# Performance work log

Hardware: AMD Instinct MI355X
Metric: run time of the kernel (lower is better)

The kernel has to match this reference:

```python
import jax, jax.numpy as jnp
import numpy as np

EPS_BN = 1e-5


def _batchnorm(h, g, b):
    # training-mode BatchNorm1d over the flattened (B*N*k) axis
    mu = jnp.mean(h, axis=0)
    var = jnp.var(h, axis=0)
    return g * (h - mu) * jax.lax.rsqrt(var + EPS_BN) + b


def setup_inputs() -> dict:
    key = jax.random.key(0)
    ks = jax.random.split(key, 5)
    B, N = 4, 8192
    x = jax.random.normal(ks[0], (B, N, 3), dtype=jnp.float32)
    W1 = jax.random.normal(ks[1], (7, 10), dtype=jnp.float32) * (1.0 / np.sqrt(7.0))
    b1 = jax.random.normal(ks[2], (10,), dtype=jnp.float32) * 0.01
    W2 = jax.random.normal(ks[3], (10, 10), dtype=jnp.float32) * (1.0 / np.sqrt(10.0))
    b2 = jax.random.normal(ks[4], (10,), dtype=jnp.float32) * 0.01
    g1 = jnp.ones((10,), jnp.float32); be1 = jnp.zeros((10,), jnp.float32)
    g2 = jnp.ones((10,), jnp.float32); be2 = jnp.zeros((10,), jnp.float32)
    return {"x": x, "W1": W1, "b1": b1, "g1": g1, "be1": be1,
            "W2": W2, "b2": b2, "g2": g2, "be2": be2, "k": 9}


def reference(x, W1, b1, g1, be1, W2, b2, g2, be2, k):
    B, N, C = x.shape
    # --- kNN graph (brute force, self included as nearest) ---
    sq = jnp.sum(x * x, axis=-1)                                    # (B,N)
    d2 = sq[:, :, None] + sq[:, None, :] - 2.0 * jnp.einsum('bnc,bmc->bnm', x, x)
    _, idx = jax.lax.top_k(-d2, k + 1)                              # (B,N,k+1)
    nbrs = x[jnp.arange(B)[:, None, None], idx]                     # (B,N,k+1,3)
    rel = (nbrs - x[:, :, None, :])[:, :, 1:, :]                    # drop self -> (B,N,k,3)
    # --- sort neighbors by azimuth phi = atan2(y, x) ---
    phi = jnp.arctan2(rel[..., 1], rel[..., 0])                     # (B,N,k)
    order = jnp.argsort(phi, axis=-1)
    v1 = jnp.take_along_axis(rel, order[..., None], axis=2)         # (B,N,k,3)
    v2 = jnp.roll(v1, -1, axis=2)                                   # next neighbor (cyclic)
    # --- umbrella-style surface features ---
    centroids = 0.5 * (v1 + v2)
    normals = jnp.cross(v1, v2)
    normals = normals / (jnp.linalg.norm(normals, axis=-1, keepdims=True) + 1e-6)
    sign = jnp.where(normals[..., 0:1, 0] > 0, 1.0, -1.0)[..., None]  # (B,N,1,1)
    normals = normals * sign
    position = jnp.sum(normals * centroids, axis=-1, keepdims=True) / jnp.sqrt(jnp.asarray(3.0, x.dtype))
    feat = jnp.concatenate([centroids, normals, position], axis=-1)   # (B,N,k,7)
    feat = feat.reshape(B * N * k, 7)
    # --- tiny MLP + max-pool over k ---
    h = jax.nn.relu(_batchnorm(feat @ W1 + b1, g1, be1))
    h = jax.nn.relu(_batchnorm(h @ W2 + b2, g2, be2))
    return jnp.max(h.reshape(B, N, k, 10), axis=2)                  # (B,N,10)
```

## Files before the change

kernel.cpp:

```cpp
#include <hip/hip_runtime.h>
#include <math.h>
#include <float.h>
#include <stdint.h>

#define B_ 4
#define N_ 8192
#define K_ 9
#define NPTS (B_ * N_)
#define NROWS (NPTS * K_)
#define SPLIT 8
#define CHUNK (N_ / SPLIT)
#define NGROUP 32
#define GSIZE (CHUNK / NGROUP)
#define GSTRIDE 33
#define NCOPY 16

typedef float f4 __attribute__((ext_vector_type(4)));
typedef float f32x2 __attribute__((ext_vector_type(2)));

__device__ __forceinline__ f32x2 dist2_pk(f32x2 xx, f32x2 yy, f32x2 zz, f32x2 ww,
                                          f32x2 qx, f32x2 qy, f32x2 qz, f32x2 qw) {
  f32x2 t0 = qx * xx;
  f32x2 t1 = __builtin_elementwise_fma(qy, yy, t0);
  f32x2 t2 = __builtin_elementwise_fma(qz, zz, t1);
  f32x2 s  = qw + ww;
  f32x2 m2 = {-2.0f, -2.0f};
  return __builtin_elementwise_fma(t2, m2, s);
}

#define GDECL(G) float gd##G; int gi##G;
#define TOURN8()                                                           \
  float e01d, e23d, e45d, e67d, f03d, f47d, md;                            \
  int   e01i, e23i, e45i, e67i, f03i, f47i, mi;                            \
  { bool t;                                                                \
    t = d1 < d0; e01d = t ? d1 : d0; e01i = t ? (j + 1) : (j + 0);         \
    t = d3 < d2; e23d = t ? d3 : d2; e23i = t ? (j + 3) : (j + 2);         \
    t = d5 < d4; e45d = t ? d5 : d4; e45i = t ? (j + 5) : (j + 4);         \
    t = d7 < d6; e67d = t ? d7 : d6; e67i = t ? (j + 7) : (j + 6);         \
    t = e23d < e01d; f03d = t ? e23d : e01d; f03i = t ? e23i : e01i;       \
    t = e67d < e45d; f47d = t ? e67d : e45d; f47i = t ? e67i : e45i;       \
    t = f47d < f03d; md = t ? f47d : f03d; mi = t ? f47i : f03i; }
#define SCANG(G)                                                           \
  { float bgd = FLT_MAX; int bgi = 0;                                      \
    _Pragma("clang loop unroll(disable)")                                  \
    for (int pr = 0; pr < 16; pr += 4) {                                   \
      const f4* cp = CH + (G * GSTRIDE + 2 * pr);                          \
      f4 A0 = cp[0], B0 = cp[1], A1 = cp[2], B1 = cp[3];                   \
      f4 A2 = cp[4], B2 = cp[5], A3 = cp[6], B3 = cp[7];                   \
      int j = G * GSIZE + 2 * pr;                                          \
      f32x2 dA = dist2_pk(__builtin_shufflevector(A0, A0, 0, 1),           \
                          __builtin_shufflevector(A0, A0, 2, 3),           \
                          __builtin_shufflevector(B0, B0, 0, 1),           \
                          __builtin_shufflevector(B0, B0, 2, 3),           \
                          qx2, qy2, qz2, qw2);                             \
      f32x2 dB = dist2_pk(__builtin_shufflevector(A1, A1, 0, 1),           \
                          __builtin_shufflevector(A1, A1, 2, 3),           \
                          __builtin_shufflevector(B1, B1, 0, 1),           \
                          __builtin_shufflevector(B1, B1, 2, 3),           \
                          qx2, qy2, qz2, qw2);                             \
      f32x2 dC = dist2_pk(__builtin_shufflevector(A2, A2, 0, 1),           \
                          __builtin_shufflevector(A2, A2, 2, 3),           \
                          __builtin_shufflevector(B2, B2, 0, 1),           \
                          __builtin_shufflevector(B2, B2, 2, 3),           \
                          qx2, qy2, qz2, qw2);                             \
      f32x2 dD = dist2_pk(__builtin_shufflevector(A3, A3, 0, 1),           \
                          __builtin_shufflevector(A3, A3, 2, 3),           \
                          __builtin_shufflevector(B3, B3, 0, 1),           \
                          __builtin_shufflevector(B3, B3, 2, 3),           \
                          qx2, qy2, qz2, qw2);                             \
      float d0 = dA.x, d1 = dA.y, d2 = dB.x, d3 = dB.y;                    \
      float d4 = dC.x, d5 = dC.y, d6 = dD.x, d7 = dD.y;                    \
      if (HS) {                                                            \
        d0 = (j + 0 == nl) ? FLT_MAX : d0;                                 \
        d1 = (j + 1 == nl) ? FLT_MAX : d1;                                 \
        d2 = (j + 2 == nl) ? FLT_MAX : d2;                                 \
        d3 = (j + 3 == nl) ? FLT_MAX : d3;                                 \
        d4 = (j + 4 == nl) ? FLT_MAX : d4;                                 \
        d5 = (j + 5 == nl) ? FLT_MAX : d5;                                 \
        d6 = (j + 6 == nl) ? FLT_MAX : d6;                                 \
        d7 = (j + 7 == nl) ? FLT_MAX : d7;                                 \
      }                                                                    \
      TOURN8();                                                            \
      bool lt = md < bgd; bgd = lt ? md : bgd; bgi = lt ? mi : bgi;        \
    }                                                                      \
    gd##G = bgd; gi##G = bgi; }
#define LMC(G, S)                                                          \
  { bool lt = gd##G < wd##S;                                               \
    wd##S = lt ? gd##G : wd##S; wi##S = lt ? gi##G : wi##S;                \
    wg##S = lt ? G : wg##S; }
#define CMB(S)                                                             \
  { bool lt = wd##S < wda;                                                 \
    wda = lt ? wd##S : wda; wia = lt ? wi##S : wia; wga = lt ? wg##S : wga; }
#define WBK(G)                                                             \
  { bool m = (wg == G); gd##G = m ? nd : gd##G; gi##G = m ? ni : gi##G; }

template <bool HS>
__device__ __forceinline__ void knn_chunk(const f4* CH, f32x2 qx2, f32x2 qy2,
                                          f32x2 qz2, f32x2 qw2,
                                          int nl, int j0, int s, int p,
                                          uint2* __restrict__ PBDI) {
  GDECL(0) GDECL(1) GDECL(2) GDECL(3) GDECL(4) GDECL(5) GDECL(6) GDECL(7)
  GDECL(8) GDECL(9) GDECL(10) GDECL(11) GDECL(12) GDECL(13) GDECL(14) GDECL(15)
  GDECL(16) GDECL(17) GDECL(18) GDECL(19) GDECL(20) GDECL(21) GDECL(22) GDECL(23)
  GDECL(24) GDECL(25) GDECL(26) GDECL(27) GDECL(28) GDECL(29) GDECL(30) GDECL(31)

  SCANG(0) SCANG(1) SCANG(2) SCANG(3) SCANG(4) SCANG(5) SCANG(6) SCANG(7)
  SCANG(8) SCANG(9) SCANG(10) SCANG(11) SCANG(12) SCANG(13) SCANG(14) SCANG(15)
  SCANG(16) SCANG(17) SCANG(18) SCANG(19) SCANG(20) SCANG(21) SCANG(22) SCANG(23)
  SCANG(24) SCANG(25) SCANG(26) SCANG(27) SCANG(28) SCANG(29) SCANG(30) SCANG(31)

#pragma clang loop unroll(disable)
  for (int r = 0; r < K_; ++r) {
    float wda = gd0; int wia = gi0; int wga = 0;
    LMC(1,a) LMC(2,a) LMC(3,a) LMC(4,a) LMC(5,a) LMC(6,a) LMC(7,a)
    float wdb = gd8; int wib = gi8; int wgb = 8;
    LMC(9,b) LMC(10,b) LMC(11,b) LMC(12,b) LMC(13,b) LMC(14,b) LMC(15,b)
    float wdc = gd16; int wic = gi16; int wgc = 16;
    LMC(17,c) LMC(18,c) LMC(19,c) LMC(20,c) LMC(21,c) LMC(22,c) LMC(23,c)
    float wdd = gd24; int wid = gi24; int wgd = 24;
    LMC(25,d) LMC(26,d) LMC(27,d) LMC(28,d) LMC(29,d) LMC(30,d) LMC(31,d)
    CMB(b) CMB(c) CMB(d)
    float wd = wda; int wi = wia; int wg = wga;

    uint2 o; o.x = __float_as_uint(wd); o.y = (unsigned)(j0 + wi);
    PBDI[(size_t)(s * K_ + r) * NPTS + p] = o;

    int ab = wg * GSTRIDE;
    int jb = wg * GSIZE;
    float nd = FLT_MAX; int ni = 0;
#pragma clang loop unroll(disable)
    for (int pr = 0; pr < 16; pr += 4) {
      const f4* cp = CH + (ab + 2 * pr);
      f4 A0 = cp[0], B0 = cp[1], A1 = cp[2], B1 = cp[3];
      f4 A2 = cp[4], B2 = cp[5], A3 = cp[6], B3 = cp[7];
      int j = jb + 2 * pr;
      f32x2 dA = dist2_pk(__builtin_shufflevector(A0, A0, 0, 1),
                          __builtin_shufflevector(A0, A0, 2, 3),
                          __builtin_shufflevector(B0, B0, 0, 1),
                          __builtin_shufflevector(B0, B0, 2, 3),
                          qx2, qy2, qz2, qw2);
      f32x2 dB = dist2_pk(__builtin_shufflevector(A1, A1, 0, 1),
                          __builtin_shufflevector(A1, A1, 2, 3),
                          __builtin_shufflevector(B1, B1, 0, 1),
                          __builtin_shufflevector(B1, B1, 2, 3),
                          qx2, qy2, qz2, qw2);
      f32x2 dC = dist2_pk(__builtin_shufflevector(A2, A2, 0, 1),
                          __builtin_shufflevector(A2, A2, 2, 3),
                          __builtin_shufflevector(B2, B2, 0, 1),
                          __builtin_shufflevector(B2, B2, 2, 3),
                          qx2, qy2, qz2, qw2);
      f32x2 dD = dist2_pk(__builtin_shufflevector(A3, A3, 0, 1),
                          __builtin_shufflevector(A3, A3, 2, 3),
                          __builtin_shufflevector(B3, B3, 0, 1),
                          __builtin_shufflevector(B3, B3, 2, 3),
                          qx2, qy2, qz2, qw2);
      float d0 = dA.x, d1 = dA.y, d2 = dB.x, d3 = dB.y;
      float d4 = dC.x, d5 = dC.y, d6 = dD.x, d7 = dD.y;
      if (HS) {
        d0 = (j + 0 == nl) ? FLT_MAX : d0;
        d1 = (j + 1 == nl) ? FLT_MAX : d1;
        d2 = (j + 2 == nl) ? FLT_MAX : d2;
        d3 = (j + 3 == nl) ? FLT_MAX : d3;
        d4 = (j + 4 == nl) ? FLT_MAX : d4;
        d5 = (j + 5 == nl) ? FLT_MAX : d5;
        d6 = (j + 6 == nl) ? FLT_MAX : d6;
        d7 = (j + 7 == nl) ? FLT_MAX : d7;
      }
      bool k0 = (d0 > wd) | ((d0 == wd) & ((j + 0) > wi));
      bool k1 = (d1 > wd) | ((d1 == wd) & ((j + 1) > wi));
      bool k2 = (d2 > wd) | ((d2 == wd) & ((j + 2) > wi));
      bool k3 = (d3 > wd) | ((d3 == wd) & ((j + 3) > wi));
      bool k4 = (d4 > wd) | ((d4 == wd) & ((j + 4) > wi));
      bool k5 = (d5 > wd) | ((d5 == wd) & ((j + 5) > wi));
      bool k6 = (d6 > wd) | ((d6 == wd) & ((j + 6) > wi));
      bool k7 = (d7 > wd) | ((d7 == wd) & ((j + 7) > wi));
      d0 = k0 ? d0 : FLT_MAX;
      d1 = k1 ? d1 : FLT_MAX;
      d2 = k2 ? d2 : FLT_MAX;
      d3 = k3 ? d3 : FLT_MAX;
      d4 = k4 ? d4 : FLT_MAX;
      d5 = k5 ? d5 : FLT_MAX;
      d6 = k6 ? d6 : FLT_MAX;
      d7 = k7 ? d7 : FLT_MAX;
      TOURN8();
      bool lt = md < nd; nd = lt ? md : nd; ni = lt ? mi : ni;
    }
    WBK(0) WBK(1) WBK(2) WBK(3) WBK(4) WBK(5) WBK(6) WBK(7)
    WBK(8) WBK(9) WBK(10) WBK(11) WBK(12) WBK(13) WBK(14) WBK(15)
    WBK(16) WBK(17) WBK(18) WBK(19) WBK(20) WBK(21) WBK(22) WBK(23)
    WBK(24) WBK(25) WBK(26) WBK(27) WBK(28) WBK(29) WBK(30) WBK(31)
  }
}

__launch_bounds__(128, 4)
__global__ void k_knn(const float* __restrict__ x, uint2* __restrict__ PBDI) {
  __shared__ f4 CH[NGROUP * GSTRIDE];
  int bid = blockIdx.x;
  int pg = bid >> 3;
  int s = bid & (SPLIT - 1);
  int p = pg * 128 + threadIdx.x;
  int b = p >> 13;
  int n = p & (N_ - 1);
  int bO = b * N_;
  int j0 = s * CHUNK;

  const float* xq = x + 3 * (size_t)p;
  float qa = xq[0], qb = xq[1], qc = xq[2];
  float qw = qa * qa + qb * qb + qc * qc;
  f32x2 qx2 = {qa, qa}, qy2 = {qb, qb}, qz2 = {qc, qc}, qw2 = {qw, qw};

  for (int u = threadIdx.x; u < CHUNK / 2; u += 128) {
    const float* xp = x + 3 * (size_t)(bO + j0 + 2 * u);
    float a0 = xp[0], b0 = xp[1], c0 = xp[2];
    float a1 = xp[3], b1 = xp[4], c1 = xp[5];
    int G = u >> 4, rr = u & 15;
    f4 lo = {a0, a1, b0, b1};
    f4 hi = {c0, c1, a0 * a0 + b0 * b0 + c0 * c0, a1 * a1 + b1 * b1 + c1 * c1};
    CH[G * GSTRIDE + 2 * rr] = lo;
    CH[G * GSTRIDE + 2 * rr + 1] = hi;
  }
  __syncthreads();

  int n0 = (pg * 128) & (N_ - 1);
  int nl = n - j0;
  if (s == (n0 >> 10)) knn_chunk<true >(CH, qx2, qy2, qz2, qw2, nl, j0, s, p, PBDI);
  else                 knn_chunk<false>(CH, qx2, qy2, qz2, qw2, nl, j0, s, p, PBDI);
}

#define LVL(bdv, biv)                                                     \
  { bool lt = cd < (bdv); float td = (bdv); int ti = (biv);               \
    (bdv) = lt ? cd : (bdv); (biv) = lt ? ci : (biv);                     \
    cd = lt ? td : cd; ci = lt ? ti : ci; }
#define INS9ALL()                                                         \
  LVL(b0d, b0i) LVL(b1d, b1i) LVL(b2d, b2i) LVL(b3d, b3i) LVL(b4d, b4i)  \
  LVL(b5d, b5i) LVL(b6d, b6i) LVL(b7d, b7i) LVL(b8d, b8i)
#define TOP9_DECL()                                                       \
  float b0d = FLT_MAX, b1d = FLT_MAX, b2d = FLT_MAX, b3d = FLT_MAX,       \
        b4d = FLT_MAX, b5d = FLT_MAX, b6d = FLT_MAX, b7d = FLT_MAX,       \
        b8d = FLT_MAX;                                                    \
  int b0i = 0, b1i = 0, b2i = 0, b3i = 0, b4i = 0, b5i = 0, b6i = 0,      \
      b7i = 0, b8i = 0;

#define MKREL(T)                                                          \
  float rx##T, ry##T, rz##T, ph##T;                                       \
  { const float* mp = x + 3 * (size_t)(bO + b##T##i);                     \
    rx##T = mp[0] - qa; ry##T = mp[1] - qb; rz##T = mp[2] - qc;           \
    ph##T = atan2f(ry##T, rx##T); }

#define CE(A, Bv)                                                         \
  { bool lt = ph##Bv < ph##A; float t0;                                   \
    t0 = ph##A; ph##A = lt ? ph##Bv : t0; ph##Bv = lt ? t0 : ph##Bv;      \
    t0 = rx##A; rx##A = lt ? rx##Bv : t0; rx##Bv = lt ? t0 : rx##Bv;      \
    t0 = ry##A; ry##A = lt ? ry##Bv : t0; ry##Bv = lt ? t0 : ry##Bv;      \
    t0 = rz##A; rz##A = lt ? rz##Bv : t0; rz##Bv = lt ? t0 : rz##Bv; }

#define ST9(arr, v0, v1, v2, v3, v4, v5, v6, v7, v8)                      \
  arr[0 * 64 + pl] = v0; arr[1 * 64 + pl] = v1; arr[2 * 64 + pl] = v2;    \
  arr[3 * 64 + pl] = v3; arr[4 * 64 + pl] = v4; arr[5 * 64 + pl] = v5;    \
  arr[6 * 64 + pl] = v6; arr[7 * 64 + pl] = v7; arr[8 * 64 + pl] = v8;

__launch_bounds__(256, 4)
__global__ void k_tail1(const float* __restrict__ x, const uint2* __restrict__ PBDI,
                        const float* __restrict__ W1, const float* __restrict__ b1,
                        float* __restrict__ H1, double* __restrict__ ACC) {
  __shared__ float  LMD[64 * 37];
  __shared__ int    LMI[64 * 37];
  __shared__ float  LREL[3][9 * 64];
  __shared__ float  LSGN[64];
  __shared__ double sred[4][20];

  int q = threadIdx.x >> 6;
  int pl = threadIdx.x & 63;
  int pbase = blockIdx.x * 64;
  int p = pbase + pl;

  {
    TOP9_DECL();
#pragma clang loop unroll_count(2)
    for (int e = 0; e < 2 * K_; ++e) {
      uint2 v = PBDI[(size_t)(q * 2 * K_ + e) * NPTS + p];
      float cd = __uint_as_float(v.x);
      int ci = (int)v.y;
      INS9ALL();
    }
    int base = pl * 37 + q * 9;
    LMD[base + 0] = b0d; LMD[base + 1] = b1d; LMD[base + 2] = b2d;
    LMD[base + 3] = b3d; LMD[base + 4] = b4d; LMD[base + 5] = b5d;
    LMD[base + 6] = b6d; LMD[base + 7] = b7d; LMD[base + 8] = b8d;
    LMI[base + 0] = b0i; LMI[base + 1] = b1i; LMI[base + 2] = b2i;
    LMI[base + 3] = b3i; LMI[base + 4] = b4i; LMI[base + 5] = b5i;
    LMI[base + 6] = b6i; LMI[base + 7] = b7i; LMI[base + 8] = b8i;
  }
  __syncthreads();

  if (q == 0) {
    int b = p >> 13;
    int bO = b * N_;
    const float* xq = x + 3 * (size_t)p;
    float qa = xq[0], qb = xq[1], qc = xq[2];

    TOP9_DECL();
#pragma clang loop unroll_count(3)
    for (int e = 0; e < 4 * K_; ++e) {
      float cd = LMD[pl * 37 + e];
      int ci = LMI[pl * 37 + e];
      INS9ALL();
    }

    MKREL(0) MKREL(1) MKREL(2) MKREL(3) MKREL(4)
    MKREL(5) MKREL(6) MKREL(7) MKREL(8)

    CE(0,1)
    CE(1,2) CE(0,1)
    CE(2,3) CE(1,2) CE(0,1)
    CE(3,4) CE(2,3) CE(1,2) CE(0,1)
    CE(4,5) CE(3,4) CE(2,3) CE(1,2) CE(0,1)
    CE(5,6) CE(4,5) CE(3,4) CE(2,3) CE(1,2) CE(0,1)
    CE(6,7) CE(5,6) CE(4,5) CE(3,4) CE(2,3) CE(1,2) CE(0,1)
    CE(7,8) CE(6,7) CE(5,6) CE(4,5) CE(3,4) CE(2,3) CE(1,2) CE(0,1)

    float nx0 = ry0 * rz1 - rz0 * ry1;
    float ny0 = rz0 * rx1 - rx0 * rz1;
    float nz0 = rx0 * ry1 - ry0 * rx1;
    float nrm0 = sqrtf(nx0 * nx0 + ny0 * ny0 + nz0 * nz0) + 1e-6f;
    LSGN[pl] = ((nx0 / nrm0) > 0.0f) ? 1.0f : -1.0f;

    ST9(LREL[0], rx0, rx1, rx2, rx3, rx4, rx5, rx6, rx7, rx8)
    ST9(LREL[1], ry0, ry1, ry2, ry3, ry4, ry5, ry6, ry7, ry8)
    ST9(LREL[2], rz0, rz1, rz2, rz3, rz4, rz5, rz6, rz7, rz8)
  }
  __syncthreads();

  double sum[10], ss[10];
#pragma unroll
  for (int c = 0; c < 10; ++c) { sum[c] = 0.0; ss[c] = 0.0; }

#pragma clang loop unroll(disable)
  for (int rl = threadIdx.x; rl < 9 * 64; rl += 256) {
    int t = rl >> 6;
    int pp = rl & 63;
    int t2 = (t + 1 == K_) ? 0 : t + 1;
    float v1x = LREL[0][t * 64 + pp];
    float v1y = LREL[1][t * 64 + pp];
    float v1z = LREL[2][t * 64 + pp];
    float v2x = LREL[0][t2 * 64 + pp];
    float v2y = LREL[1][t2 * 64 + pp];
    float v2z = LREL[2][t2 * 64 + pp];
    float sgn = LSGN[pp];

    float cx = 0.5f * (v1x + v2x);
    float cy = 0.5f * (v1y + v2y);
    float cz = 0.5f * (v1z + v2z);
    float nx = v1y * v2z - v1z * v2y;
    float ny = v1z * v2x - v1x * v2z;
    float nz = v1x * v2y - v1y * v2x;
    float nrm = sqrtf(nx * nx + ny * ny + nz * nz) + 1e-6f;
    nx /= nrm; ny /= nrm; nz /= nrm;
    nx *= sgn; ny *= sgn; nz *= sgn;
    float pos = (nx * cx + ny * cy + nz * cz) / 1.7320508075688772f;

    float fv[7] = {cx, cy, cz, nx, ny, nz, pos};
#pragma unroll
    for (int c = 0; c < 10; ++c) {
      float h = b1[c];
#pragma unroll
      for (int rr = 0; rr < 7; ++rr) h = fmaf(fv[rr], W1[rr * 10 + c], h);
      H1[(size_t)c * NROWS + (size_t)t * NPTS + pbase + pp] = h;
      double hd = (double)h;
      sum[c] += hd; ss[c] += hd * hd;
    }
  }

  int lane = threadIdx.x & 63, wv = threadIdx.x >> 6;
#pragma unroll
  for (int c = 0; c < 10; ++c) {
    double a = sum[c];
#pragma unroll
    for (int off = 32; off > 0; off >>= 1) a += __shfl_down(a, off);
    if (lane == 0) sred[wv][c] = a;
    double qq = ss[c];
#pragma unroll
    for (int off = 32; off > 0; off >>= 1) qq += __shfl_down(qq, off);
    if (lane == 0) sred[wv][10 + c] = qq;
  }
  __syncthreads();
  if (threadIdx.x < 20) {
    atomicAdd(&ACC[(blockIdx.x & (NCOPY - 1)) * 40 + threadIdx.x],
              sred[0][threadIdx.x] + sred[1][threadIdx.x] +
              sred[2][threadIdx.x] + sred[3][threadIdx.x]);
  }
}

__launch_bounds__(256)
__global__ void k_mlp2(const float* __restrict__ H1, double* __restrict__ ACC,
                       const float* __restrict__ g1, const float* __restrict__ be1,
                       const float* __restrict__ W2, const float* __restrict__ b2,
                       float* __restrict__ H2) {
  __shared__ float MR[20];
  if (threadIdx.x < 10) {
    double s0 = 0.0, s1 = 0.0;
#pragma unroll
    for (int cc = 0; cc < NCOPY; ++cc) {
      s0 += ACC[cc * 40 + threadIdx.x];
      s1 += ACC[cc * 40 + 10 + threadIdx.x];
    }
    double mu = s0 / (double)NROWS;
    double var = s1 / (double)NROWS - mu * mu;
    MR[threadIdx.x] = (float)mu;
    MR[10 + threadIdx.x] = (float)(1.0 / sqrt(var + 1e-5));
  }
  __syncthreads();

  int r = blockIdx.x * 256 + threadIdx.x;
  float v[10];
#pragma unroll
  for (int c = 0; c < 10; ++c) {
    float h = H1[(size_t)c * NROWS + r];
    float z = g1[c] * (h - MR[c]) * MR[10 + c] + be1[c];
    v[c] = z > 0.0f ? z : 0.0f;
  }
  float o[10];
#pragma unroll
  for (int c = 0; c < 10; ++c) {
    float h = b2[c];
#pragma unroll
    for (int t = 0; t < 10; ++t) h = fmaf(v[t], W2[t * 10 + c], h);
    o[c] = h;
    H2[(size_t)c * NROWS + r] = h;
  }

  __shared__ double sred[4][20];
  int lane = threadIdx.x & 63, wv = threadIdx.x >> 6;
#pragma unroll
  for (int c = 0; c < 10; ++c) {
    double a = (double)o[c];
#pragma unroll
    for (int off = 32; off > 0; off >>= 1) a += __shfl_down(a, off);
    if (lane == 0) sred[wv][c] = a;
    double qq = (double)o[c] * (double)o[c];
#pragma unroll
    for (int off = 32; off > 0; off >>= 1) qq += __shfl_down(qq, off);
    if (lane == 0) sred[wv][10 + c] = qq;
  }
  __syncthreads();
  if (threadIdx.x < 20) {
    atomicAdd(&ACC[(blockIdx.x & (NCOPY - 1)) * 40 + 20 + threadIdx.x],
              sred[0][threadIdx.x] + sred[1][threadIdx.x] +
              sred[2][threadIdx.x] + sred[3][threadIdx.x]);
  }
}

__launch_bounds__(256)
__global__ void k_out(const float* __restrict__ H2, const double* __restrict__ ACC,
                      const float* __restrict__ g2, const float* __restrict__ be2,
                      float* __restrict__ out) {
  __shared__ float MR[20];
  if (threadIdx.x < 10) {
    double s0 = 0.0, s1 = 0.0;
#pragma unroll
    for (int cc = 0; cc < NCOPY; ++cc) {
      s0 += ACC[cc * 40 + 20 + threadIdx.x];
      s1 += ACC[cc * 40 + 30 + threadIdx.x];
    }
    double mu = s0 / (double)NROWS;
    double var = s1 / (double)NROWS - mu * mu;
    MR[threadIdx.x] = (float)mu;
    MR[10 + threadIdx.x] = (float)(1.0 / sqrt(var + 1e-5));
  }
  __syncthreads();

  int p = blockIdx.x * 256 + threadIdx.x;
#pragma unroll
  for (int c = 0; c < 10; ++c) {
    float m = -FLT_MAX;
#pragma unroll
    for (int j = 0; j < K_; ++j) {
      float h = H2[(size_t)c * NROWS + j * NPTS + p];
      float z = g2[c] * (h - MR[c]) * MR[10 + c] + be2[c];
      z = z > 0.0f ? z : 0.0f;
      m = fmaxf(m, z);
    }
    out[(size_t)p * 10 + c] = m;
  }
}

extern "C" void kernel_launch(void* const* d_in, const int* in_sizes, int n_in,
                              void* d_out, int out_size, void* d_ws, size_t ws_size,
                              hipStream_t stream) {
  (void)in_sizes; (void)n_in; (void)out_size; (void)ws_size;
  const float* x  = (const float*)d_in[0];
  const float* W1 = (const float*)d_in[1];
  const float* b1 = (const float*)d_in[2];
  const float* g1 = (const float*)d_in[3];
  const float* be1= (const float*)d_in[4];
  const float* W2 = (const float*)d_in[5];
  const float* b2 = (const float*)d_in[6];
  const float* g2 = (const float*)d_in[7];
  const float* be2= (const float*)d_in[8];
  float* out = (float*)d_out;

  char* base = (char*)d_ws;
  uint2*  PBDI = (uint2*)base;
  float*  H1 = (float*)(base + (size_t)SPLIT * K_ * NPTS * 8);
  double* ACC = (double*)(H1 + (size_t)10 * NROWS);
  float*  H2 = (float*)PBDI;

  hipMemsetAsync(ACC, 0, NCOPY * 40 * sizeof(double), stream);
  k_knn<<<(NPTS / 128) * SPLIT, 128, 0, stream>>>(x, PBDI);
  k_tail1<<<NPTS / 64, 256, 0, stream>>>(x, PBDI, W1, b1, H1, ACC);
  k_mlp2<<<NROWS / 256, 256, 0, stream>>>(H1, ACC, g1, be1, W2, b2, H2);
  k_out<<<NPTS / 256, 256, 0, stream>>>(H2, ACC, g2, be2, out);
}
```

Baseline: 236.5 us.

## Drop index tracking from kNN group scan and cache winner-group distances in registers

The first-pass group scan now keeps only the minimum distance per group, using fminf with no index tournament. In each extraction round the winning group's distances are recomputed once into 32 registers. The index is recovered as the lowest index matching the minimum, and the refill tournament reuses those cached values instead of a second LDS pass. The output kernel is also relaunched with 64-thread blocks, and the BN-statistics setup is split across 20 threads. This cuts ALU work in the dominant scan, at the cost of register pressure and extra compare work in each round.

```diff
diff --git a/kernel.cpp b/kernel.cpp
--- a/kernel.cpp
+++ b/kernel.cpp
@@ -18,6 +18,9 @@
 typedef float f4 __attribute__((ext_vector_type(4)));
 typedef float f32x2 __attribute__((ext_vector_type(2)));
 
+#define SH(V, a, b) __builtin_shufflevector(V, V, a, b)
+#define IMIN(a, b) (((a) < (b)) ? (a) : (b))
+
 __device__ __forceinline__ f32x2 dist2_pk(f32x2 xx, f32x2 yy, f32x2 zz, f32x2 ww,
                                           f32x2 qx, f32x2 qy, f32x2 qz, f32x2 qw) {
   f32x2 t0 = qx * xx;
@@ -29,6 +32,91 @@
 }
 
 #define GDECL(G) float gd##G; int gi##G;
+
+#define SCANG(G)                                                           \
+  { float bgd = FLT_MAX;                                                   \
+    _Pragma("clang loop unroll(disable)")                                  \
+    for (int pr = 0; pr < 16; pr += 4) {                                   \
+      const f4* cp = CH + (G * GSTRIDE + 2 * pr);                          \
+      f4 A0 = cp[0], B0 = cp[1], A1 = cp[2], B1 = cp[3];                   \
+      f4 A2 = cp[4], B2 = cp[5], A3 = cp[6], B3 = cp[7];                   \
+      f32x2 dA = dist2_pk(SH(A0,0,1), SH(A0,2,3), SH(B0,0,1), SH(B0,2,3),  \
+                          qx2, qy2, qz2, qw2);                             \
+      f32x2 dB = dist2_pk(SH(A1,0,1), SH(A1,2,3), SH(B1,0,1), SH(B1,2,3),  \
+                          qx2, qy2, qz2, qw2);                             \
+      f32x2 dC = dist2_pk(SH(A2,0,1), SH(A2,2,3), SH(B2,0,1), SH(B2,2,3),  \
+                          qx2, qy2, qz2, qw2);                             \
+      f32x2 dD = dist2_pk(SH(A3,0,1), SH(A3,2,3), SH(B3,0,1), SH(B3,2,3),  \
+                          qx2, qy2, qz2, qw2);                             \
+      float d0 = dA.x, d1 = dA.y, d2 = dB.x, d3 = dB.y;                    \
+      float d4 = dC.x, d5 = dC.y, d6 = dD.x, d7 = dD.y;                    \
+      if (HS) {                                                            \
+        int j = G * GSIZE + 2 * pr;                                        \
+        d0 = (j + 0 == nl) ? FLT_MAX : d0;                                 \
+        d1 = (j + 1 == nl) ? FLT_MAX : d1;                                 \
+        d2 = (j + 2 == nl) ? FLT_MAX : d2;                                 \
+        d3 = (j + 3 == nl) ? FLT_MAX : d3;                                 \
+        d4 = (j + 4 == nl) ? FLT_MAX : d4;                                 \
+        d5 = (j + 5 == nl) ? FLT_MAX : d5;                                 \
+        d6 = (j + 6 == nl) ? FLT_MAX : d6;                                 \
+        d7 = (j + 7 == nl) ? FLT_MAX : d7;                                 \
+      }                                                                    \
+      float m = fminf(fminf(fminf(d0, d1), fminf(d2, d3)),                 \
+                      fminf(fminf(d4, d5), fminf(d6, d7)));                \
+      bgd = fminf(bgd, m);                                                 \
+    }                                                                      \
+    gd##G = bgd; gi##G = -1; }
+
+#define LMC(G, S)                                                          \
+  { bool lt = gd##G < wd##S;                                               \
+    wd##S = lt ? gd##G : wd##S; wi##S = lt ? gi##G : wi##S;                \
+    wg##S = lt ? G : wg##S; }
+#define CMB(S)                                                             \
+  { bool lt = wd##S < wda;                                                 \
+    wda = lt ? wd##S : wda; wia = lt ? wi##S : wia; wga = lt ? wg##S : wga; }
+#define WBK(G)                                                             \
+  { bool m = (wg == G); gd##G = m ? nd : gd##G; gi##G = m ? ni : gi##G; }
+
+#define RESC(T, OFS)                                                       \
+  { const f4* cp = CH + (ab + OFS);                                        \
+    f4 A0 = cp[0], B0 = cp[1], A1 = cp[2], B1 = cp[3];                     \
+    f4 A2 = cp[4], B2 = cp[5], A3 = cp[6], B3 = cp[7];                     \
+    f32x2 dA = dist2_pk(SH(A0,0,1), SH(A0,2,3), SH(B0,0,1), SH(B0,2,3),    \
+                        qx2, qy2, qz2, qw2);                               \
+    f32x2 dB = dist2_pk(SH(A1,0,1), SH(A1,2,3), SH(B1,0,1), SH(B1,2,3),    \
+                        qx2, qy2, qz2, qw2);                               \
+    f32x2 dC = dist2_pk(SH(A2,0,1), SH(A2,2,3), SH(B2,0,1), SH(B2,2,3),    \
+                        qx2, qy2, qz2, qw2);                               \
+    f32x2 dD = dist2_pk(SH(A3,0,1), SH(A3,2,3), SH(B3,0,1), SH(B3,2,3),    \
+                        qx2, qy2, qz2, qw2);                               \
+    rc##T##0 = dA.x; rc##T##1 = dA.y; rc##T##2 = dB.x; rc##T##3 = dB.y;    \
+    rc##T##4 = dC.x; rc##T##5 = dC.y; rc##T##6 = dD.x; rc##T##7 = dD.y;    \
+    if (HS) {                                                              \
+      int j = jb + OFS;                                                    \
+      rc##T##0 = (j + 0 == nl) ? FLT_MAX : rc##T##0;                       \
+      rc##T##1 = (j + 1 == nl) ? FLT_MAX : rc##T##1;                       \
+      rc##T##2 = (j + 2 == nl) ? FLT_MAX : rc##T##2;                       \
+      rc##T##3 = (j + 3 == nl) ? FLT_MAX : rc##T##3;                       \
+      rc##T##4 = (j + 4 == nl) ? FLT_MAX : rc##T##4;                       \
+      rc##T##5 = (j + 5 == nl) ? FLT_MAX : rc##T##5;                       \
+      rc##T##6 = (j + 6 == nl) ? FLT_MAX : rc##T##6;                       \
+      rc##T##7 = (j + 7 == nl) ? FLT_MAX : rc##T##7;                       \
+    } }
+
+#define MT8(T, OFS)                                                        \
+  { int j = jb + OFS;                                                      \
+    int a0 = (rc##T##0 == wd) ? (j + 0) : 0x7fffffff;                      \
+    int a1 = (rc##T##1 == wd) ? (j + 1) : 0x7fffffff;                      \
+    int a2 = (rc##T##2 == wd) ? (j + 2) : 0x7fffffff;                      \
+    int a3 = (rc##T##3 == wd) ? (j + 3) : 0x7fffffff;                      \
+    int a4 = (rc##T##4 == wd) ? (j + 4) : 0x7fffffff;                      \
+    int a5 = (rc##T##5 == wd) ? (j + 5) : 0x7fffffff;                      \
+    int a6 = (rc##T##6 == wd) ? (j + 6) : 0x7fffffff;                      \
+    int a7 = (rc##T##7 == wd) ? (j + 7) : 0x7fffffff;                      \
+    int mA = IMIN(IMIN(a0, a1), IMIN(a2, a3));                             \
+    int mB = IMIN(IMIN(a4, a5), IMIN(a6, a7));                             \
+    jm = IMIN(jm, IMIN(mA, mB)); }
+
 #define TOURN8()                                                           \
   float e01d, e23d, e45d, e67d, f03d, f47d, md;                            \
   int   e01i, e23i, e45i, e67i, f03i, f47i, mi;                            \
@@ -40,59 +128,29 @@
     t = e23d < e01d; f03d = t ? e23d : e01d; f03i = t ? e23i : e01i;       \
     t = e67d < e45d; f47d = t ? e67d : e45d; f47i = t ? e67i : e45i;       \
     t = f47d < f03d; md = t ? f47d : f03d; mi = t ? f47i : f03i; }
-#define SCANG(G)                                                           \
-  { float bgd = FLT_MAX; int bgi = 0;                                      \
-    _Pragma("clang loop unroll(disable)")                                  \
-    for (int pr = 0; pr < 16; pr += 4) {                                   \
-      const f4* cp = CH + (G * GSTRIDE + 2 * pr);                          \
-      f4 A0 = cp[0], B0 = cp[1], A1 = cp[2], B1 = cp[3];                   \
-      f4 A2 = cp[4], B2 = cp[5], A3 = cp[6], B3 = cp[7];                   \
-      int j = G * GSIZE + 2 * pr;                                          \
-      f32x2 dA = dist2_pk(__builtin_shufflevector(A0, A0, 0, 1),           \
-                          __builtin_shufflevector(A0, A0, 2, 3),           \
-                          __builtin_shufflevector(B0, B0, 0, 1),           \
-                          __builtin_shufflevector(B0, B0, 2, 3),           \
-                          qx2, qy2, qz2, qw2);                             \
-      f32x2 dB = dist2_pk(__builtin_shufflevector(A1, A1, 0, 1),           \
-                          __builtin_shufflevector(A1, A1, 2, 3),           \
-                          __builtin_shufflevector(B1, B1, 0, 1),           \
-                          __builtin_shufflevector(B1, B1, 2, 3),           \
-                          qx2, qy2, qz2, qw2);                             \
-      f32x2 dC = dist2_pk(__builtin_shufflevector(A2, A2, 0, 1),           \
-                          __builtin_shufflevector(A2, A2, 2, 3),           \
-                          __builtin_shufflevector(B2, B2, 0, 1),           \
-                          __builtin_shufflevector(B2, B2, 2, 3),           \
-                          qx2, qy2, qz2, qw2);                             \
-      f32x2 dD = dist2_pk(__builtin_shufflevector(A3, A3, 0, 1),           \
-                          __builtin_shufflevector(A3, A3, 2, 3),           \
-                          __builtin_shufflevector(B3, B3, 0, 1),           \
-                          __builtin_shufflevector(B3, B3, 2, 3),           \
-                          qx2, qy2, qz2, qw2);                             \
-      float d0 = dA.x, d1 = dA.y, d2 = dB.x, d3 = dB.y;                    \
-      float d4 = dC.x, d5 = dC.y, d6 = dD.x, d7 = dD.y;                    \
-      if (HS) {                                                            \
-        d0 = (j + 0 == nl) ? FLT_MAX : d0;                                 \
-        d1 = (j + 1 == nl) ? FLT_MAX : d1;                                 \
-        d2 = (j + 2 == nl) ? FLT_MAX : d2;                                 \
-        d3 = (j + 3 == nl) ? FLT_MAX : d3;                                 \
-        d4 = (j + 4 == nl) ? FLT_MAX : d4;                                 \
-        d5 = (j + 5 == nl) ? FLT_MAX : d5;                                 \
-        d6 = (j + 6 == nl) ? FLT_MAX : d6;                                 \
-        d7 = (j + 7 == nl) ? FLT_MAX : d7;                                 \
-      }                                                                    \
-      TOURN8();                                                            \
-      bool lt = md < bgd; bgd = lt ? md : bgd; bgi = lt ? mi : bgi;        \
-    }                                                                      \
-    gd##G = bgd; gi##G = bgi; }
-#define LMC(G, S)                                                          \
-  { bool lt = gd##G < wd##S;                                               \
-    wd##S = lt ? gd##G : wd##S; wi##S = lt ? gi##G : wi##S;                \
-    wg##S = lt ? G : wg##S; }
-#define CMB(S)                                                             \
-  { bool lt = wd##S < wda;                                                 \
-    wda = lt ? wd##S : wda; wia = lt ? wi##S : wia; wga = lt ? wg##S : wga; }
-#define WBK(G)                                                             \
-  { bool m = (wg == G); gd##G = m ? nd : gd##G; gi##G = m ? ni : gi##G; }
+
+#define RF(T, OFS)                                                         \
+  { float d0 = rc##T##0, d1 = rc##T##1, d2 = rc##T##2, d3 = rc##T##3;      \
+    float d4 = rc##T##4, d5 = rc##T##5, d6 = rc##T##6, d7 = rc##T##7;      \
+    int j = jb + OFS;                                                      \
+    bool k0 = (d0 > wd) | ((d0 == wd) & ((j + 0) > wi));                   \
+    bool k1 = (d1 > wd) | ((d1 == wd) & ((j + 1) > wi));                   \
+    bool k2 = (d2 > wd) | ((d2 == wd) & ((j + 2) > wi));                   \
+    bool k3 = (d3 > wd) | ((d3 == wd) & ((j + 3) > wi));                   \
+    bool k4 = (d4 > wd) | ((d4 == wd) & ((j + 4) > wi));                   \
+    bool k5 = (d5 > wd) | ((d5 == wd) & ((j + 5) > wi));                   \
+    bool k6 = (d6 > wd) | ((d6 == wd) & ((j + 6) > wi));                   \
+    bool k7 = (d7 > wd) | ((d7 == wd) & ((j + 7) > wi));                   \
+    d0 = k0 ? d0 : FLT_MAX;                                                \
+    d1 = k1 ? d1 : FLT_MAX;                                                \
+    d2 = k2 ? d2 : FLT_MAX;                                                \
+    d3 = k3 ? d3 : FLT_MAX;                                                \
+    d4 = k4 ? d4 : FLT_MAX;                                                \
+    d5 = k5 ? d5 : FLT_MAX;                                                \
+    d6 = k6 ? d6 : FLT_MAX;                                                \
+    d7 = k7 ? d7 : FLT_MAX;                                                \
+    TOURN8();                                                              \
+    bool lt = md < nd; nd = lt ? md : nd; ni = lt ? mi : ni; }
 
 template <bool HS>
 __device__ __forceinline__ void knn_chunk(const f4* CH, f32x2 qx2, f32x2 qy2,
@@ -120,71 +178,27 @@
     float wdd = gd24; int wid = gi24; int wgd = 24;
     LMC(25,d) LMC(26,d) LMC(27,d) LMC(28,d) LMC(29,d) LMC(30,d) LMC(31,d)
     CMB(b) CMB(c) CMB(d)
-    float wd = wda; int wi = wia; int wg = wga;
+    float wd = wda; int wist = wia; int wg = wga;
+
+    int ab = wg * GSTRIDE;
+    int jb = wg * GSIZE;
+
+    float rcA0, rcA1, rcA2, rcA3, rcA4, rcA5, rcA6, rcA7;
+    float rcB0, rcB1, rcB2, rcB3, rcB4, rcB5, rcB6, rcB7;
+    float rcC0, rcC1, rcC2, rcC3, rcC4, rcC5, rcC6, rcC7;
+    float rcD0, rcD1, rcD2, rcD3, rcD4, rcD5, rcD6, rcD7;
+    RESC(A, 0) RESC(B, 8) RESC(C, 16) RESC(D, 24)
+
+    int jm = 0x7fffffff;
+    MT8(A, 0) MT8(B, 8) MT8(C, 16) MT8(D, 24)
+    int wi = (wist >= 0) ? wist : jm;
 
     uint2 o; o.x = __float_as_uint(wd); o.y = (unsigned)(j0 + wi);
     PBDI[(size_t)(s * K_ + r) * NPTS + p] = o;
 
-    int ab = wg * GSTRIDE;
-    int jb = wg * GSIZE;
     float nd = FLT_MAX; int ni = 0;
-#pragma clang loop unroll(disable)
-    for (int pr = 0; pr < 16; pr += 4) {
-      const f4* cp = CH + (ab + 2 * pr);
-      f4 A0 = cp[0], B0 = cp[1], A1 = cp[2], B1 = cp[3];
-      f4 A2 = cp[4], B2 = cp[5], A3 = cp[6], B3 = cp[7];
-      int j = jb + 2 * pr;
-      f32x2 dA = dist2_pk(__builtin_shufflevector(A0, A0, 0, 1),
-                          __builtin_shufflevector(A0, A0, 2, 3),
-                          __builtin_shufflevector(B0, B0, 0, 1),
-                          __builtin_shufflevector(B0, B0, 2, 3),
-                          qx2, qy2, qz2, qw2);
-      f32x2 dB = dist2_pk(__builtin_shufflevector(A1, A1, 0, 1),
-                          __builtin_shufflevector(A1, A1, 2, 3),
-                          __builtin_shufflevector(B1, B1, 0, 1),
-                          __builtin_shufflevector(B1, B1, 2, 3),
-                          qx2, qy2, qz2, qw2);
-      f32x2 dC = dist2_pk(__builtin_shufflevector(A2, A2, 0, 1),
-                          __builtin_shufflevector(A2, A2, 2, 3),
-                          __builtin_shufflevector(B2, B2, 0, 1),
-                          __builtin_shufflevector(B2, B2, 2, 3),
-                          qx2, qy2, qz2, qw2);
-      f32x2 dD = dist2_pk(__builtin_shufflevector(A3, A3, 0, 1),
-                          __builtin_shufflevector(A3, A3, 2, 3),
-                          __builtin_shufflevector(B3, B3, 0, 1),
-                          __builtin_shufflevector(B3, B3, 2, 3),
-                          qx2, qy2, qz2, qw2);
-      float d0 = dA.x, d1 = dA.y, d2 = dB.x, d3 = dB.y;
-      float d4 = dC.x, d5 = dC.y, d6 = dD.x, d7 = dD.y;
-      if (HS) {
-        d0 = (j + 0 == nl) ? FLT_MAX : d0;
-        d1 = (j + 1 == nl) ? FLT_MAX : d1;
-        d2 = (j + 2 == nl) ? FLT_MAX : d2;
-        d3 = (j + 3 == nl) ? FLT_MAX : d3;
-        d4 = (j + 4 == nl) ? FLT_MAX : d4;
-        d5 = (j + 5 == nl) ? FLT_MAX : d5;
-        d6 = (j + 6 == nl) ? FLT_MAX : d6;
-        d7 = (j + 7 == nl) ? FLT_MAX : d7;
-      }
-      bool k0 = (d0 > wd) | ((d0 == wd) & ((j + 0) > wi));
-      bool k1 = (d1 > wd) | ((d1 == wd) & ((j + 1) > wi));
-      bool k2 = (d2 > wd) | ((d2 == wd) & ((j + 2) > wi));
-      bool k3 = (d3 > wd) | ((d3 == wd) & ((j + 3) > wi));
-      bool k4 = (d4 > wd) | ((d4 == wd) & ((j + 4) > wi));
-      bool k5 = (d5 > wd) | ((d5 == wd) & ((j + 5) > wi));
-      bool k6 = (d6 > wd) | ((d6 == wd) & ((j + 6) > wi));
-      bool k7 = (d7 > wd) | ((d7 == wd) & ((j + 7) > wi));
-      d0 = k0 ? d0 : FLT_MAX;
-      d1 = k1 ? d1 : FLT_MAX;
-      d2 = k2 ? d2 : FLT_MAX;
-      d3 = k3 ? d3 : FLT_MAX;
-      d4 = k4 ? d4 : FLT_MAX;
-      d5 = k5 ? d5 : FLT_MAX;
-      d6 = k6 ? d6 : FLT_MAX;
-      d7 = k7 ? d7 : FLT_MAX;
-      TOURN8();
-      bool lt = md < nd; nd = lt ? md : nd; ni = lt ? mi : ni;
-    }
+    RF(A, 0) RF(B, 8) RF(C, 16) RF(D, 24)
+
     WBK(0) WBK(1) WBK(2) WBK(3) WBK(4) WBK(5) WBK(6) WBK(7)
     WBK(8) WBK(9) WBK(10) WBK(11) WBK(12) WBK(13) WBK(14) WBK(15)
     WBK(16) WBK(17) WBK(18) WBK(19) WBK(20) WBK(21) WBK(22) WBK(23)
@@ -450,26 +464,27 @@
   }
 }
 
-__launch_bounds__(256)
+__launch_bounds__(64)
 __global__ void k_out(const float* __restrict__ H2, const double* __restrict__ ACC,
                       const float* __restrict__ g2, const float* __restrict__ be2,
                       float* __restrict__ out) {
   __shared__ float MR[20];
-  if (threadIdx.x < 10) {
+  if (threadIdx.x < 20) {
+    int c = threadIdx.x % 10;
+    int half = threadIdx.x / 10;
     double s0 = 0.0, s1 = 0.0;
 #pragma unroll
     for (int cc = 0; cc < NCOPY; ++cc) {
-      s0 += ACC[cc * 40 + 20 + threadIdx.x];
-      s1 += ACC[cc * 40 + 30 + threadIdx.x];
+      s0 += ACC[cc * 40 + 20 + c];
+      s1 += ACC[cc * 40 + 30 + c];
     }
     double mu = s0 / (double)NROWS;
     double var = s1 / (double)NROWS - mu * mu;
-    MR[threadIdx.x] = (float)mu;
-    MR[10 + threadIdx.x] = (float)(1.0 / sqrt(var + 1e-5));
-  }
-  __syncthreads();
-
-  int p = blockIdx.x * 256 + threadIdx.x;
+    MR[threadIdx.x] = half ? (float)(1.0 / sqrt(var + 1e-5)) : (float)mu;
+  }
+  __syncthreads();
+
+  int p = blockIdx.x * 64 + threadIdx.x;
 #pragma unroll
   for (int c = 0; c < 10; ++c) {
     float m = -FLT_MAX;
@@ -509,5 +524,5 @@
   k_knn<<<(NPTS / 128) * SPLIT, 128, 0, stream>>>(x, PBDI);
   k_tail1<<<NPTS / 64, 256, 0, stream>>>(x, PBDI, W1, b1, H1, ACC);
   k_mlp2<<<NROWS / 256, 256, 0, stream>>>(H1, ACC, g1, be1, W2, b2, H2);
-  k_out<<<NPTS / 256, 256, 0, stream>>>(H2, ACC, g2, be2, out);
-}
+  k_out<<<NPTS / 64, 64, 0, stream>>>(H2, ACC, g2, be2, out);
+}
```

Result: no change. 235.7 us (-0.3%).

## Reduce max over k before second BatchNorm using monotonicity and gamma sign

Applied to the files above, without the earlier changes.

k_mlp2 now processes one point per thread, iterates over its k neighbor rows, and keeps a running max (or min when gamma2 is negative) of the pre-BN layer-2 outputs. Only these per-point extremes are written, instead of the full k-row H2 tensor. k_out then applies BN+ReLU to a single value per channel. This relies on BN+ReLU being monotone in h with direction set by the sign of gamma, and it removes most of the H2 write and reread traffic. The cost is smaller 64-thread blocks and a serial per-thread loop over k.

```diff
diff --git a/kernel.cpp b/kernel.cpp
--- a/kernel.cpp
+++ b/kernel.cpp
@@ -391,96 +391,107 @@
   }
 }
 
-__launch_bounds__(256)
+__launch_bounds__(64)
 __global__ void k_mlp2(const float* __restrict__ H1, double* __restrict__ ACC,
                        const float* __restrict__ g1, const float* __restrict__ be1,
                        const float* __restrict__ W2, const float* __restrict__ b2,
-                       float* __restrict__ H2) {
+                       const float* __restrict__ g2, float* __restrict__ EXT) {
   __shared__ float MR[20];
-  if (threadIdx.x < 10) {
+  __shared__ double sred[20];
+  if (threadIdx.x < 20) {
+    int c = threadIdx.x % 10;
+    int half = threadIdx.x / 10;
     double s0 = 0.0, s1 = 0.0;
 #pragma unroll
     for (int cc = 0; cc < NCOPY; ++cc) {
-      s0 += ACC[cc * 40 + threadIdx.x];
-      s1 += ACC[cc * 40 + 10 + threadIdx.x];
+      s0 += ACC[cc * 40 + c];
+      s1 += ACC[cc * 40 + 10 + c];
     }
     double mu = s0 / (double)NROWS;
     double var = s1 / (double)NROWS - mu * mu;
-    MR[threadIdx.x] = (float)mu;
-    MR[10 + threadIdx.x] = (float)(1.0 / sqrt(var + 1e-5));
-  }
-  __syncthreads();
-
-  int r = blockIdx.x * 256 + threadIdx.x;
-  float v[10];
+    MR[threadIdx.x] = half ? (float)(1.0 / sqrt(var + 1e-5)) : (float)mu;
+  }
+  __syncthreads();
+
+  int p = blockIdx.x * 64 + threadIdx.x;
+  double sum[10], ss[10];
+  float ext[10], sg[10];
 #pragma unroll
   for (int c = 0; c < 10; ++c) {
-    float h = H1[(size_t)c * NROWS + r];
-    float z = g1[c] * (h - MR[c]) * MR[10 + c] + be1[c];
-    v[c] = z > 0.0f ? z : 0.0f;
-  }
-  float o[10];
+    sum[c] = 0.0; ss[c] = 0.0;
+    sg[c] = g2[c];
+    ext[c] = (sg[c] >= 0.0f) ? -FLT_MAX : FLT_MAX;
+  }
+
+#pragma clang loop unroll(disable)
+  for (int t = 0; t < K_; ++t) {
+    float v[10];
+#pragma unroll
+    for (int c = 0; c < 10; ++c) {
+      float h = H1[(size_t)c * NROWS + (size_t)t * NPTS + p];
+      float z = g1[c] * (h - MR[c]) * MR[10 + c] + be1[c];
+      v[c] = z > 0.0f ? z : 0.0f;
+    }
+#pragma unroll
+    for (int c = 0; c < 10; ++c) {
+      float h = b2[c];
+#pragma unroll
+      for (int u = 0; u < 10; ++u) h = fmaf(v[u], W2[u * 10 + c], h);
+      sum[c] += (double)h;
+      ss[c] += (double)h * (double)h;
+      ext[c] = (sg[c] >= 0.0f) ? fmaxf(ext[c], h) : fminf(ext[c], h);
+    }
+  }
+
+#pragma unroll
+  for (int c = 0; c < 10; ++c)
+    EXT[(size_t)c * NPTS + p] = ext[c];
+
 #pragma unroll
   for (int c = 0; c < 10; ++c) {
-    float h = b2[c];
-#pragma unroll
-    for (int t = 0; t < 10; ++t) h = fmaf(v[t], W2[t * 10 + c], h);
-    o[c] = h;
-    H2[(size_t)c * NROWS + r] = h;
-  }
-
-  __shared__ double sred[4][20];
-  int lane = threadIdx.x & 63, wv = threadIdx.x >> 6;
-#pragma unroll
-  for (int c = 0; c < 10; ++c) {
-    double a = (double)o[c];
+    double a = sum[c];
 #pragma unroll
     for (int off = 32; off > 0; off >>= 1) a += __shfl_down(a, off);
-    if (lane == 0) sred[wv][c] = a;
-    double qq = (double)o[c] * (double)o[c];
+    if (threadIdx.x == 0) sred[c] = a;
+    double qq = ss[c];
 #pragma unroll
     for (int off = 32; off > 0; off >>= 1) qq += __shfl_down(qq, off);
-    if (lane == 0) sred[wv][10 + c] = qq;
+    if (threadIdx.x == 0) sred[10 + c] = qq;
   }
   __syncthreads();
   if (threadIdx.x < 20) {
     atomicAdd(&ACC[(blockIdx.x & (NCOPY - 1)) * 40 + 20 + threadIdx.x],
-              sred[0][threadIdx.x] + sred[1][threadIdx.x] +
-              sred[2][threadIdx.x] + sred[3][threadIdx.x]);
-  }
-}
-
-__launch_bounds__(256)
-__global__ void k_out(const float* __restrict__ H2, const double* __restrict__ ACC,
+              sred[threadIdx.x]);
+  }
+}
+
+__launch_bounds__(64)
+__global__ void k_out(const float* __restrict__ EXT, const double* __restrict__ ACC,
                       const float* __restrict__ g2, const float* __restrict__ be2,
                       float* __restrict__ out) {
   __shared__ float MR[20];
-  if (threadIdx.x < 10) {
+  if (threadIdx.x < 20) {
+    int c = threadIdx.x % 10;
+    int half = threadIdx.x / 10;
     double s0 = 0.0, s1 = 0.0;
 #pragma unroll
     for (int cc = 0; cc < NCOPY; ++cc) {
-      s0 += ACC[cc * 40 + 20 + threadIdx.x];
-      s1 += ACC[cc * 40 + 30 + threadIdx.x];
+      s0 += ACC[cc * 40 + 20 + c];
+      s1 += ACC[cc * 40 + 30 + c];
     }
     double mu = s0 / (double)NROWS;
     double var = s1 / (double)NROWS - mu * mu;
-    MR[threadIdx.x] = (float)mu;
-    MR[10 + threadIdx.x] = (float)(1.0 / sqrt(var + 1e-5));
-  }
-  __syncthreads();
-
-  int p = blockIdx.x * 256 + threadIdx.x;
+    MR[threadIdx.x] = half ? (float)(1.0 / sqrt(var + 1e-5)) : (float)mu;
+  }
+  __syncthreads();
+
+  int p = blockIdx.x * 64 + threadIdx.x;
 #pragma unroll
   for (int c = 0; c < 10; ++c) {
-    float m = -FLT_MAX;
-#pragma unroll
-    for (int j = 0; j < K_; ++j) {
-      float h = H2[(size_t)c * NROWS + j * NPTS + p];
-      float z = g2[c] * (h - MR[c]) * MR[10 + c] + be2[c];
-      z = z > 0.0f ? z : 0.0f;
-      m = fmaxf(m, z);
-    }
-    out[(size_t)p * 10 + c] = m;
+    float h = EXT[(size_t)c * NPTS + p];
+    float z = g2[c] * (h - MR[c]) * MR[10 + c] + be2[c];
+    z = z > 0.0f ? z : 0.0f;
+    out[(size_t)p * 10 + c] = z;
   }
 }
 
@@ -503,11 +514,11 @@
   uint2*  PBDI = (uint2*)base;
   float*  H1 = (float*)(base + (size_t)SPLIT * K_ * NPTS * 8);
   double* ACC = (double*)(H1 + (size_t)10 * NROWS);
-  float*  H2 = (float*)PBDI;
+  float*  EXT = (float*)PBDI;
 
   hipMemsetAsync(ACC, 0, NCOPY * 40 * sizeof(double), stream);
   k_knn<<<(NPTS / 128) * SPLIT, 128, 0, stream>>>(x, PBDI);
   k_tail1<<<NPTS / 64, 256, 0, stream>>>(x, PBDI, W1, b1, H1, ACC);
-  k_mlp2<<<NROWS / 256, 256, 0, stream>>>(H1, ACC, g1, be1, W2, b2, H2);
-  k_out<<<NPTS / 256, 256, 0, stream>>>(H2, ACC, g2, be2, out);
-}
+  k_mlp2<<<NPTS / 64, 64, 0, stream>>>(H1, ACC, g1, be1, W2, b2, g2, EXT);
+  k_out<<<NPTS / 64, 64, 0, stream>>>(EXT, ACC, g2, be2, out);
+}
```

Result: faster. 231.6 us (-2.1%).
